# Kernel optimization log

Measured on AMD Instinct MI355X. Metric: run time of the kernel, lower is better.

## Reference

```python
import jax, jax.numpy as jnp
import numpy as np

N_NODES = 50000
N_EDGES = 1600000
N_GRAPHS = 512
D_IN, H1, H2, D_EMB = 128, 256, 256, 128
EPS = 1e-5


def setup_inputs() -> dict:
    key = jax.random.key(0)
    ks = jax.random.split(key, 12)
    V = jax.random.normal(ks[0], (N_NODES, D_IN), dtype=jnp.float32)
    edge_index = jax.random.randint(ks[1], (2, N_EDGES), 0, N_NODES, dtype=jnp.int64)
    batch_ids = jnp.sort(jax.random.randint(ks[2], (N_NODES,), 0, N_GRAPHS, dtype=jnp.int64))
    s = 0.05
    return {
        "V": V,
        "edge_index": edge_index,
        "batch_ids": batch_ids,
        "W1": jax.random.normal(ks[3], (D_IN, H1), jnp.float32) * s,
        "b1": jnp.zeros((H1,), jnp.float32),
        "g1": jnp.ones((H1,), jnp.float32),
        "be1": jnp.zeros((H1,), jnp.float32),
        "W2": jax.random.normal(ks[4], (H1, H2), jnp.float32) * s,
        "b2": jnp.zeros((H2,), jnp.float32),
        "g2": jnp.ones((H2,), jnp.float32),
        "be2": jnp.zeros((H2,), jnp.float32),
        "Wfc": jax.random.normal(ks[5], (H2, D_EMB), jnp.float32) * s,
        "bfc": jnp.zeros((D_EMB,), jnp.float32),
    }


def _gcn_conv(x, W, b, src, dst, n_nodes):
    x = x @ W  # [N, h]
    deg = jax.ops.segment_sum(jnp.ones_like(dst, dtype=x.dtype), dst, num_segments=n_nodes)
    dinv = jnp.where(deg > 0, jax.lax.rsqrt(deg), jnp.zeros_like(deg))
    norm = dinv[src] * dinv[dst]  # [E+N]
    out = jax.ops.segment_sum(x[src] * norm[:, None], dst, num_segments=n_nodes)
    return out + b


def _batch_norm(x, gamma, beta):
    mean = x.mean(axis=0)
    var = x.var(axis=0)  # biased, matches torch BN training normalization
    return (x - mean) * jax.lax.rsqrt(var + EPS) * gamma + beta


def reference(V, edge_index, batch_ids, W1, b1, g1, be1, W2, b2, g2, be2, Wfc, bfc):
    n = V.shape[0]
    loops = jnp.arange(n, dtype=edge_index.dtype)
    src = jnp.concatenate([edge_index[0], loops])
    dst = jnp.concatenate([edge_index[1], loops])

    h = _gcn_conv(V, W1, b1, src, dst, n)
    h = jax.nn.relu(_batch_norm(h, g1, be1))
    h = _gcn_conv(h, W2, b2, src, dst, n)
    h = jax.nn.relu(_batch_norm(h, g2, be2))

    # global mean pool over graphs
    sums = jax.ops.segment_sum(h, batch_ids, num_segments=N_GRAPHS)
    counts = jax.ops.segment_sum(jnp.ones((n,), h.dtype), batch_ids, num_segments=N_GRAPHS)
    G = sums / jnp.maximum(counts, 1.0)[:, None]
    return G @ Wfc + bfc
```

## Files before the change

kernel.cpp:

```cpp
#include <hip/hip_runtime.h>
#include <stdint.h>

typedef unsigned int u32;
typedef unsigned short u16;
typedef unsigned char u8;
typedef __attribute__((ext_vector_type(8))) short short8;
typedef __attribute__((ext_vector_type(4))) float f32x4;
typedef __attribute__((ext_vector_type(2))) float f32x2;

#if !__has_builtin(__builtin_amdgcn_cvt_pk_f32_fp8) || !__has_builtin(__builtin_amdgcn_cvt_pk_fp8_f32)
#include <hip/hip_fp8.h>
#define FP8_FALLBACK 1
#endif

#define NN   50000
#define NPAD 50048
#define NG   512
#define DIN  128
#define DH   256
#define BN_EPS 1e-5f
#define NB   196
#define EPB  4096
#define WCAP 24576
#define NT   8
#define TDIV 6250

#define CAST_BLK 6250
#define WT1_BLK  128
#define WT2_BLK  256

__device__ __forceinline__ float bf2f(u16 u) {
  union { u32 i; float f; } v; v.i = ((u32)u) << 16; return v.f;
}
__device__ __forceinline__ float bflo(u32 p) {
  union { u32 i; float f; } v; v.i = p << 16; return v.f;
}
__device__ __forceinline__ float bfhi(u32 p) {
  union { u32 i; float f; } v; v.i = p & 0xFFFF0000u; return v.f;
}
__device__ __forceinline__ u16 f2bf(float f) {
  union { float f; u32 i; } v; v.f = f;
  return (u16)((v.i + 0x7FFFu + ((v.i >> 16) & 1u)) >> 16);
}
__device__ __forceinline__ int load_idx(const void* p, long long i, int is64) {
  return is64 ? (int)((const long long*)p)[i] : ((const int*)p)[i];
}

__device__ __forceinline__ void fp8x4_dec(u32 w, float* o) {
#ifndef FP8_FALLBACK
  f32x2 lo = __builtin_amdgcn_cvt_pk_f32_fp8(w, false);
  f32x2 hi = __builtin_amdgcn_cvt_pk_f32_fp8(w, true);
  o[0] = lo.x; o[1] = lo.y; o[2] = hi.x; o[3] = hi.y;
#else
  __hip_fp8_e4m3 t;
#pragma unroll
  for (int k = 0; k < 4; ++k) { t.__x = (u8)(w >> (8 * k)); o[k] = (float)t; }
#endif
}
__device__ __forceinline__ u32 fp8x4_enc(float a, float b, float c, float d) {
#ifndef FP8_FALLBACK
  u32 r = 0;
  r = __builtin_amdgcn_cvt_pk_fp8_f32(a, b, r, false);
  r = __builtin_amdgcn_cvt_pk_fp8_f32(c, d, r, true);
  return r;
#else
  __hip_fp8_e4m3 qa(a), qb(b), qc(c), qd(d);
  return (u32)qa.__x | ((u32)qb.__x << 8) | ((u32)qc.__x << 16) | ((u32)qd.__x << 24);
#endif
}

__global__ void k_detect(const int* ei, int* flag) {
  if (threadIdx.x == 0 && blockIdx.x == 0) {
    int oddz = 0;
    for (int i = 0; i < 128; ++i) oddz += (ei[2 * i + 1] == 0) ? 1 : 0;
    *flag = (oddz == 128) ? 1 : 0;
  }
}

__global__ __launch_bounds__(256) void k_bcnt(const void* ei, int E,
    int* __restrict__ bcnt, const int* flag) {
  __shared__ int h[NB];
  int is64 = *flag;
  int t = threadIdx.x;
  for (int i = t; i < NB; i += 256) h[i] = 0;
  __syncthreads();
  long long base = (long long)blockIdx.x * EPB + t * 16;
#pragma unroll
  for (int j = 0; j < 16; ++j) {
    long long e = base + j;
    if (e < E) {
      int d = load_idx(ei, (long long)E + e, is64);
      atomicAdd(&h[d >> 8], 1);
    }
  }
  __syncthreads();
  for (int i = t; i < NB; i += 256)
    if (h[i]) atomicAdd(&bcnt[i], h[i]);
}

__global__ void k_bscan(const int* __restrict__ bcnt, int* __restrict__ bbase,
                        int* __restrict__ bcur) {
  __shared__ int s[256];
  int t = threadIdx.x;
  s[t] = (t < NB) ? bcnt[t] : 0; __syncthreads();
  for (int off = 1; off < 256; off <<= 1) {
    int x = s[t];
    int y = (t >= off) ? s[t - off] : 0;
    __syncthreads();
    s[t] = x + y; __syncthreads();
  }
  if (t < NB) {
    int ex = (t == 0) ? 0 : s[t - 1];
    bbase[t] = ex;
    bcur[t] = ex;
  }
}

__global__ __launch_bounds__(256) void k_bfill(const void* ei, int E,
    int* __restrict__ bcur, u32* __restrict__ recs, const int* flag) {
  __shared__ int h[NB];
  __shared__ int lbase[NB];
  __shared__ int lcur[NB];
  int is64 = *flag;
  int t = threadIdx.x;
  for (int i = t; i < NB; i += 256) h[i] = 0;
  __syncthreads();
  u32 rr[16];
  int bb[16];
  long long base = (long long)blockIdx.x * EPB + t * 16;
#pragma unroll
  for (int j = 0; j < 16; ++j) {
    long long e = base + j;
    if (e < E) {
      int s = load_idx(ei, e, is64);
      int d = load_idx(ei, (long long)E + e, is64);
      int b = d >> 8;
      rr[j] = ((u32)s << 8) | (u32)(d & 255);
      bb[j] = b;
      atomicAdd(&h[b], 1);
    } else bb[j] = -1;
  }
  __syncthreads();
  for (int i = t; i < NB; i += 256) {
    lbase[i] = h[i] ? atomicAdd(&bcur[i], h[i]) : 0;
    lcur[i] = 0;
  }
  __syncthreads();
#pragma unroll
  for (int j = 0; j < 16; ++j) {
    if (bb[j] >= 0) {
      int loc = atomicAdd(&lcur[bb[j]], 1);
      recs[lbase[bb[j]] + loc] = rr[j];
    }
  }
}

__global__ __launch_bounds__(512) void k_build(const u32* __restrict__ recs,
    const int* __restrict__ bbase, const int* __restrict__ bcnt,
    int* __restrict__ deg, int* __restrict__ offs, float* __restrict__ dinv,
    u16* __restrict__ csr_s) {
  __shared__ u32 cnt2[256][NT];
  __shared__ int woff[256];
  __shared__ int sscan[256];
  __shared__ u16 stage[WCAP];
  int b = blockIdx.x;
  int t = threadIdx.x;
  int nodeBase = b * 256;
  int nin = min(256, NN - nodeBase);
  for (int i = t; i < 256 * NT; i += 512) ((u32*)cnt2)[i] = 0;
  __syncthreads();
  int rb = bbase[b], cnt = bcnt[b];
  for (int i = t; i < cnt; i += 512) {
    u32 r = recs[rb + i];
    atomicAdd(&cnt2[r & 255u][(r >> 8) / TDIV], 1u);
  }
  __syncthreads();
  int slots = 0;
  if (t < nin) {
    cnt2[t][(u32)(nodeBase + t) / TDIV] += 1u;
    u32 run = 0;
#pragma unroll
    for (int k = 0; k < NT; ++k) { u32 c = cnt2[t][k]; cnt2[t][k] = run; run += c; }
    slots = (int)run;
  }
  if (t < 256) sscan[t] = slots;
  __syncthreads();
  for (int off = 1; off < 256; off <<= 1) {
    int x = (t < 256) ? sscan[t] : 0;
    int y = (t >= off && t < 256) ? sscan[t - off] : 0;
    __syncthreads();
    if (t < 256) sscan[t] = x + y;
    __syncthreads();
  }
  int gbase = rb + nodeBase;
  if (t < nin) {
    int ex = sscan[t] - slots;
    woff[t] = ex;
    offs[nodeBase + t] = gbase + ex;
    deg[nodeBase + t] = slots - 1;
    dinv[nodeBase + t] = rsqrtf((float)slots);
  }
  __syncthreads();
  int winsize = cnt + nin;
  if (winsize <= WCAP) {
    for (int i = t; i < cnt; i += 512) {
      u32 r = recs[rb + i];
      int d = r & 255u;
      u32 src = r >> 8;
      int loc = (int)atomicAdd(&cnt2[d][src / TDIV], 1u);
      stage[woff[d] + loc] = (u16)src;
    }
    if (t < nin) {
      int loc = (int)atomicAdd(&cnt2[t][(u32)(nodeBase + t) / TDIV], 1u);
      stage[woff[t] + loc] = (u16)(nodeBase + t);
    }
    __syncthreads();
    for (int i = t; i < winsize; i += 512) csr_s[gbase + i] = stage[i];
  } else {
    for (int i = t; i < cnt; i += 512) {
      u32 r = recs[rb + i];
      int d = r & 255u;
      u32 src = r >> 8;
      int loc = (int)atomicAdd(&cnt2[d][src / TDIV], 1u);
      csr_s[gbase + woff[d] + loc] = (u16)src;
    }
    if (t < nin) {
      int loc = (int)atomicAdd(&cnt2[t][(u32)(nodeBase + t) / TDIV], 1u);
      csr_s[gbase + woff[t] + loc] = (u16)(nodeBase + t);
    }
  }
}

__global__ void k_prep(const float* __restrict__ V, const float* __restrict__ W1,
                       const float* __restrict__ W2, const float* __restrict__ dinv,
                       u16* __restrict__ Vb, u16* __restrict__ W1t,
                       u16* __restrict__ W2t) {
  int b = blockIdx.x;
  if (b < CAST_BLK) {
    int i = (b * 256 + threadIdx.x) * 4;
    float dv = dinv[i >> 7];
    float4 v = *(const float4*)(V + i);
    ushort4 o;
    o.x = f2bf(v.x * dv); o.y = f2bf(v.y * dv);
    o.z = f2bf(v.z * dv); o.w = f2bf(v.w * dv);
    *(ushort4*)(Vb + i) = o;
  } else if (b < CAST_BLK + WT1_BLK) {
    int i = (b - CAST_BLK) * 256 + threadIdx.x;
    int k = i >> 8, c = i & 255;
    W1t[c * DIN + k] = f2bf(W1[i]);
  } else {
    int i = (b - CAST_BLK - WT1_BLK) * 256 + threadIdx.x;
    int k = i >> 8, c = i & 255;
    W2t[c * DH + k] = f2bf(W2[i]);
  }
}

__global__ __launch_bounds__(256) void k_agg1(const u16* __restrict__ in,
    const int* __restrict__ offs, const int* __restrict__ deg,
    const u16* __restrict__ csr_s, const float* __restrict__ dinv,
    u16* __restrict__ out) {
  int node = (blockIdx.x * 256 + threadIdx.x) >> 6;
  int lane = threadIdx.x & 63;
  if (node >= NN) return;
  int beg = offs[node];
  int end = beg + deg[node] + 1;
  float dinvn = dinv[node];
  int grp = lane >> 4, sub = lane & 15;
  float acc[8] = {};
  int e = beg + grp;
  bool v0 = e < end, v1 = e + 4 < end, v2 = e + 8 < end;
  uint4 r0, r1, r2;
  if (v0) r0 = *((const uint4*)(in + (size_t)csr_s[e] * 128) + sub);
  if (v1) r1 = *((const uint4*)(in + (size_t)csr_s[e + 4] * 128) + sub);
  if (v2) r2 = *((const uint4*)(in + (size_t)csr_s[e + 8] * 128) + sub);
  e += 12;
  while (v0) {
    bool v3 = e < end;
    uint4 r3;
    if (v3) r3 = *((const uint4*)(in + (size_t)csr_s[e] * 128) + sub);
    {
      u32 w[4] = {r0.x, r0.y, r0.z, r0.w};
#pragma unroll
      for (int j = 0; j < 4; ++j) {
        acc[2 * j + 0] += bflo(w[j]);
        acc[2 * j + 1] += bfhi(w[j]);
      }
    }
    r0 = r1; r1 = r2; r2 = r3;
    v0 = v1; v1 = v2; v2 = v3;
    e += 4;
  }
#pragma unroll
  for (int j = 0; j < 8; ++j) {
    acc[j] += __shfl_xor(acc[j], 16, 64);
    acc[j] += __shfl_xor(acc[j], 32, 64);
  }
  if (lane < 16) {
    u16* op = out + (size_t)node * 128 + sub * 8;
#pragma unroll
    for (int q = 0; q < 2; ++q) {
      ushort4 o;
      o.x = f2bf(acc[4 * q + 0] * dinvn);
      o.y = f2bf(acc[4 * q + 1] * dinvn);
      o.z = f2bf(acc[4 * q + 2] * dinvn);
      o.w = f2bf(acc[4 * q + 3] * dinvn);
      *(ushort4*)(op + 4 * q) = o;
    }
  }
}

__global__ __launch_bounds__(256) void k_agg2(const u8* __restrict__ in,
    const int* __restrict__ offs, const int* __restrict__ deg,
    const u16* __restrict__ csr_s, const float* __restrict__ dinv,
    u16* __restrict__ out) {
  int node = (blockIdx.x * 256 + threadIdx.x) >> 6;
  int lane = threadIdx.x & 63;
  if (node >= NN) return;
  int beg = offs[node];
  int end = beg + deg[node] + 1;
  float dinvn = dinv[node];
  int grp = lane >> 4, sub = lane & 15;
  float acc[16] = {};
  int e = beg + grp;
  bool v0 = e < end, v1 = e + 4 < end, v2 = e + 8 < end;
  uint4 r0, r1, r2;
  if (v0) r0 = *((const uint4*)(in + (size_t)csr_s[e] * 256) + sub);
  if (v1) r1 = *((const uint4*)(in + (size_t)csr_s[e + 4] * 256) + sub);
  if (v2) r2 = *((const uint4*)(in + (size_t)csr_s[e + 8] * 256) + sub);
  e += 12;
  while (v0) {
    bool v3 = e < end;
    uint4 r3;
    if (v3) r3 = *((const uint4*)(in + (size_t)csr_s[e] * 256) + sub);
    {
      u32 w[4] = {r0.x, r0.y, r0.z, r0.w};
#pragma unroll
      for (int j = 0; j < 4; ++j) {
        float f[4];
        fp8x4_dec(w[j], f);
        acc[4 * j + 0] += f[0];
        acc[4 * j + 1] += f[1];
        acc[4 * j + 2] += f[2];
        acc[4 * j + 3] += f[3];
      }
    }
    r0 = r1; r1 = r2; r2 = r3;
    v0 = v1; v1 = v2; v2 = v3;
    e += 4;
  }
#pragma unroll
  for (int j = 0; j < 16; ++j) {
    acc[j] += __shfl_xor(acc[j], 16, 64);
    acc[j] += __shfl_xor(acc[j], 32, 64);
  }
  if (lane < 16) {
    u16* op = out + (size_t)node * 256 + sub * 16;
#pragma unroll
    for (int q = 0; q < 4; ++q) {
      ushort4 o;
      o.x = f2bf(acc[4 * q + 0] * dinvn);
      o.y = f2bf(acc[4 * q + 1] * dinvn);
      o.z = f2bf(acc[4 * q + 2] * dinvn);
      o.w = f2bf(acc[4 * q + 3] * dinvn);
      *(ushort4*)(op + 4 * q) = o;
    }
  }
}

__global__ __launch_bounds__(256) void k_mgemm(const u16* __restrict__ A,
    const u16* __restrict__ Bt, const float* __restrict__ bias,
    u16* __restrict__ out, int M, int K,
    float* __restrict__ sums, float* __restrict__ sumsq) {
  __shared__ __align__(16) u16 As[128 * 32];
  __shared__ __align__(16) u16 Bs[128 * 32];
  int t = threadIdx.x;
  int l = t & 63;
  int w = t >> 6;
  int rowBase = blockIdx.x * 128;
  int colBase = blockIdx.y * 128;
  int wr = (w >> 1) * 64, wc = (w & 1) * 64;
  int rsel = l & 15, ksel = (l >> 4) * 8;

  f32x4 acc[4][4];
#pragma unroll
  for (int mi = 0; mi < 4; ++mi)
#pragma unroll
    for (int ni = 0; ni < 4; ++ni) acc[mi][ni] = (f32x4){0.f, 0.f, 0.f, 0.f};

  for (int k0 = 0; k0 < K; k0 += 32) {
#pragma unroll
    for (int c = 0; c < 2; ++c) {
      int idx = c * 256 + t;
      int row = idx >> 2;
      int kq = idx & 3;
      const u16* ga = A + (size_t)(rowBase + row) * K + k0 + kq * 8;
      const u16* gb = Bt + (size_t)(colBase + row) * K + k0 + kq * 8;
      __builtin_amdgcn_global_load_lds(
          (const __attribute__((address_space(1))) void*)ga,
          (__attribute__((address_space(3))) void*)(&As[idx * 8]), 16, 0, 0);
      __builtin_amdgcn_global_load_lds(
          (const __attribute__((address_space(1))) void*)gb,
          (__attribute__((address_space(3))) void*)(&Bs[idx * 8]), 16, 0, 0);
    }
    __syncthreads();
    short8 a[4], b[4];
#pragma unroll
    for (int mi = 0; mi < 4; ++mi)
      a[mi] = *(const short8*)(&As[(wr + mi * 16 + rsel) * 32 + ksel]);
#pragma unroll
    for (int ni = 0; ni < 4; ++ni)
      b[ni] = *(const short8*)(&Bs[(wc + ni * 16 + rsel) * 32 + ksel]);
#pragma unroll
    for (int mi = 0; mi < 4; ++mi)
#pragma unroll
      for (int ni = 0; ni < 4; ++ni)
        acc[mi][ni] = __builtin_amdgcn_mfma_f32_16x16x32_bf16(a[mi], b[ni], acc[mi][ni], 0, 0, 0);
    __syncthreads();
  }

#pragma unroll
  for (int ni = 0; ni < 4; ++ni) {
    int col = colBase + wc + ni * 16 + (l & 15);
    float bcol = bias[col];
    float s1 = 0.f, s2 = 0.f;
#pragma unroll
    for (int mi = 0; mi < 4; ++mi) {
#pragma unroll
      for (int r = 0; r < 4; ++r) {
        int row = rowBase + wr + mi * 16 + (l >> 4) * 4 + r;
        if (row < M) {
          float v = acc[mi][ni][r] + bcol;
          s1 += v; s2 += v * v;
          out[(size_t)row * 256 + col] = f2bf(v);
        }
      }
    }
    s1 += __shfl_xor(s1, 16, 64); s1 += __shfl_xor(s1, 32, 64);
    s2 += __shfl_xor(s2, 16, 64); s2 += __shfl_xor(s2, 32, 64);
    if (l < 16) {
      atomicAdd(&sums[col], s1);
      atomicAdd(&sumsq[col], s2);
    }
  }
}

__global__ void k_scale(const float* __restrict__ sum, const float* __restrict__ sumsq,
                        const float* __restrict__ g, const float* __restrict__ be,
                        float* __restrict__ scale, float* __restrict__ shift) {
  int c = threadIdx.x;
  float mean = sum[c] / (float)NN;
  float var = sumsq[c] / (float)NN - mean * mean;
  float sc = g[c] * rsqrtf(var + BN_EPS);
  scale[c] = sc;
  shift[c] = be[c] - mean * sc;
}

__global__ __launch_bounds__(256) void k_normcast(const u16* __restrict__ h,
    const float* __restrict__ scale, const float* __restrict__ shift,
    const float* __restrict__ dinv, u32* __restrict__ y) {
  long long i = ((long long)blockIdx.x * 256 + threadIdx.x) * 8;
  int row = (int)(i >> 8);
  float dv = dinv[row];
  int c = (int)(i & 255);
  ushort4 v0 = *(const ushort4*)(h + i);
  ushort4 v1 = *(const ushort4*)(h + i + 4);
  float f[8];
  f[0] = fmaxf(bf2f(v0.x) * scale[c + 0] + shift[c + 0], 0.f) * dv;
  f[1] = fmaxf(bf2f(v0.y) * scale[c + 1] + shift[c + 1], 0.f) * dv;
  f[2] = fmaxf(bf2f(v0.z) * scale[c + 2] + shift[c + 2], 0.f) * dv;
  f[3] = fmaxf(bf2f(v0.w) * scale[c + 3] + shift[c + 3], 0.f) * dv;
  f[4] = fmaxf(bf2f(v1.x) * scale[c + 4] + shift[c + 4], 0.f) * dv;
  f[5] = fmaxf(bf2f(v1.y) * scale[c + 5] + shift[c + 5], 0.f) * dv;
  f[6] = fmaxf(bf2f(v1.z) * scale[c + 6] + shift[c + 6], 0.f) * dv;
  f[7] = fmaxf(bf2f(v1.w) * scale[c + 7] + shift[c + 7], 0.f) * dv;
  uint2 o;
  o.x = fp8x4_enc(f[0], f[1], f[2], f[3]);
  o.y = fp8x4_enc(f[4], f[5], f[6], f[7]);
  *(uint2*)(y + (i >> 2)) = o;
}

__global__ __launch_bounds__(256) void k_pool(const u16* __restrict__ h,
    const float* __restrict__ scale, const float* __restrict__ shift,
    const void* batch, float* __restrict__ Gsum, int* __restrict__ Gcnt,
    const int* flag) {
  int is64 = *flag;
  int c = threadIdx.x;
  int nodeBase = blockIdx.x * 64;
  float sc = scale[c], sh = shift[c];
  float local = 0.f;
  int cur = -1, len = 0;
  int nmax = min(64, NN - nodeBase);
  for (int r = 0; r < nmax; ++r) {
    int node = nodeBase + r;
    int b = load_idx(batch, node, is64);
    if (b != cur) {
      if (cur >= 0) {
        atomicAdd(&Gsum[(size_t)cur * 256 + c], local);
        if (c == 0) atomicAdd(&Gcnt[cur], len);
      }
      cur = b; local = 0.f; len = 0;
    }
    float v = bf2f(h[(size_t)node * 256 + c]) * sc + sh;
    local += fmaxf(v, 0.f);
    len++;
  }
  if (cur >= 0) {
    atomicAdd(&Gsum[(size_t)cur * 256 + c], local);
    if (c == 0) atomicAdd(&Gcnt[cur], len);
  }
}

__global__ __launch_bounds__(128) void k_fc(const float* __restrict__ Gsum,
    const int* __restrict__ Gcnt, const float* __restrict__ Wfc,
    const float* __restrict__ bfc, float* __restrict__ out) {
  int g = blockIdx.x, j = threadIdx.x;
  float inv = 1.0f / fmaxf((float)Gcnt[g], 1.0f);
  float acc = 0.f;
#pragma unroll 4
  for (int c = 0; c < 256; ++c) acc += Gsum[(size_t)g * 256 + c] * Wfc[c * 128 + j];
  out[(size_t)g * 128 + j] = acc * inv + bfc[j];
}

extern "C" void kernel_launch(void* const* d_in, const int* in_sizes, int n_in,
                              void* d_out, int out_size, void* d_ws, size_t ws_size,
                              hipStream_t stream) {
  const float* V   = (const float*)d_in[0];
  const void*  EI  = d_in[1];
  const void*  BAT = d_in[2];
  const float* W1  = (const float*)d_in[3];
  const float* b1  = (const float*)d_in[4];
  const float* g1  = (const float*)d_in[5];
  const float* be1 = (const float*)d_in[6];
  const float* W2  = (const float*)d_in[7];
  const float* b2  = (const float*)d_in[8];
  const float* g2  = (const float*)d_in[9];
  const float* be2 = (const float*)d_in[10];
  const float* Wfc = (const float*)d_in[11];
  const float* bfc = (const float*)d_in[12];
  float* out = (float*)d_out;
  const int E  = in_sizes[1] / 2;
  const int NE = E + NN;

  char* w = (char*)d_ws;
  size_t o = 0;
  auto alloc = [&](size_t bytes) -> char* {
    char* r = w + o;
    o = (o + bytes + 255) & ~(size_t)255;
    return r;
  };
  int*   flag   = (int*)alloc(4);
  int*   deg    = (int*)alloc((size_t)NN * 4);
  int*   offs   = (int*)alloc((size_t)NN * 4);
  int*   bcnt   = (int*)alloc(NB * 4);
  int*   bbase  = (int*)alloc(NB * 4);
  int*   bcur   = (int*)alloc(NB * 4);
  u32*   recs   = (u32*)alloc((size_t)E * 4);
  u16*   csr_s  = (u16*)alloc((size_t)NE * 2);
  float* dinv   = (float*)alloc((size_t)NN * 4);
  float* stats  = (float*)alloc(8 * 256 * 4);
  float *sums1 = stats, *sumsq1 = stats + 256, *sums2 = stats + 512, *sumsq2 = stats + 768;
  float *scale1 = stats + 1024, *shift1 = stats + 1280, *scale2 = stats + 1536, *shift2 = stats + 1792;
  float* Gsum   = (float*)alloc((size_t)NG * DH * 4);
  int*   Gcnt   = (int*)alloc(NG * 4);
  u16*   W1t    = (u16*)alloc((size_t)256 * DIN * 2);
  u16*   W2t    = (u16*)alloc((size_t)256 * DH * 2);
  u16*   Vb     = (u16*)alloc((size_t)NN * DIN * 2);
  u16*   agg1   = (u16*)alloc((size_t)NPAD * DIN * 2);
  u16*   h1b    = (u16*)alloc((size_t)NN * DH * 2);
  u32*   h1n8   = (u32*)alloc((size_t)NN * DH);
  u16*   agg2   = (u16*)alloc((size_t)NPAD * DH * 2);
  u16*   h2b    = (u16*)alloc((size_t)NN * DH * 2);
  (void)n_in; (void)out_size; (void)ws_size;

  hipMemsetAsync(bcnt, 0, NB * 4, stream);
  hipMemsetAsync(stats, 0, 4 * 256 * 4, stream);
  hipMemsetAsync(Gsum, 0, (size_t)NG * DH * 4, stream);
  hipMemsetAsync(Gcnt, 0, (size_t)NG * 4, stream);

  const int gB = (E + EPB - 1) / EPB;

  k_detect<<<1, 64, 0, stream>>>((const int*)EI, flag);
  k_bcnt<<<gB, 256, 0, stream>>>(EI, E, bcnt, flag);
  k_bscan<<<1, 256, 0, stream>>>(bcnt, bbase, bcur);
  k_bfill<<<gB, 256, 0, stream>>>(EI, E, bcur, recs, flag);
  k_build<<<NB, 512, 0, stream>>>(recs, bbase, bcnt, deg, offs, dinv, csr_s);
  k_prep<<<CAST_BLK + WT1_BLK + WT2_BLK, 256, 0, stream>>>(V, W1, W2, dinv, Vb, W1t, W2t);

  k_agg1<<<(NN + 3) / 4, 256, 0, stream>>>(Vb, offs, deg, csr_s, dinv, agg1);
  k_mgemm<<<dim3((NN + 127) / 128, 2), 256, 0, stream>>>(agg1, W1t, b1, h1b, NN, DIN,
                                                         sums1, sumsq1);
  k_scale<<<1, 256, 0, stream>>>(sums1, sumsq1, g1, be1, scale1, shift1);
  k_normcast<<<6250, 256, 0, stream>>>(h1b, scale1, shift1, dinv, h1n8);

  k_agg2<<<(NN + 3) / 4, 256, 0, stream>>>((const u8*)h1n8, offs, deg, csr_s, dinv, agg2);
  k_mgemm<<<dim3((NN + 127) / 128, 2), 256, 0, stream>>>(agg2, W2t, b2, h2b, NN, DH,
                                                         sums2, sumsq2);
  k_scale<<<1, 256, 0, stream>>>(sums2, sumsq2, g2, be2, scale2, shift2);

  k_pool<<<(NN + 63) / 64, 256, 0, stream>>>(h2b, scale2, shift2, BAT, Gsum, Gcnt, flag);
  k_fc<<<NG, 128, 0, stream>>>(Gsum, Gcnt, Wfc, bfc, out);
}
```

Baseline: 336.9 us.

## Store layer-1 gathered features as FP8 and retile CSR source-ordering buckets

The input features, prescaled by dinv, are now stored as FP8 e4m3 instead of bf16, which halves the bytes the layer-1 aggregation gathers per edge. The agg1 kernel is reorganised so each 8-lane group covers a full 128-byte row and 8 edges are processed in parallel, with one extra shuffle stage in the reduction. Separately, the CSR build parameters change from 8 to 16 source tiles with a smaller window capacity, which alters how neighbour lists are ordered for locality. The cost is lower precision in the first aggregation, which risks accuracy error.

```diff
diff --git a/kernel.cpp b/kernel.cpp
--- a/kernel.cpp
+++ b/kernel.cpp
@@ -21,9 +21,9 @@
 #define BN_EPS 1e-5f
 #define NB   196
 #define EPB  4096
-#define WCAP 24576
-#define NT   8
-#define TDIV 6250
+#define WCAP 16384
+#define NT   16
+#define TDIV 3125
 
 #define CAST_BLK 6250
 #define WT1_BLK  128
@@ -31,12 +31,6 @@
 
 __device__ __forceinline__ float bf2f(u16 u) {
   union { u32 i; float f; } v; v.i = ((u32)u) << 16; return v.f;
-}
-__device__ __forceinline__ float bflo(u32 p) {
-  union { u32 i; float f; } v; v.i = p << 16; return v.f;
-}
-__device__ __forceinline__ float bfhi(u32 p) {
-  union { u32 i; float f; } v; v.i = p & 0xFFFF0000u; return v.f;
 }
 __device__ __forceinline__ u16 f2bf(float f) {
   union { float f; u32 i; } v; v.f = f;
@@ -233,17 +227,14 @@
 
 __global__ void k_prep(const float* __restrict__ V, const float* __restrict__ W1,
                        const float* __restrict__ W2, const float* __restrict__ dinv,
-                       u16* __restrict__ Vb, u16* __restrict__ W1t,
+                       u32* __restrict__ Vb8, u16* __restrict__ W1t,
                        u16* __restrict__ W2t) {
   int b = blockIdx.x;
   if (b < CAST_BLK) {
     int i = (b * 256 + threadIdx.x) * 4;
     float dv = dinv[i >> 7];
     float4 v = *(const float4*)(V + i);
-    ushort4 o;
-    o.x = f2bf(v.x * dv); o.y = f2bf(v.y * dv);
-    o.z = f2bf(v.z * dv); o.w = f2bf(v.w * dv);
-    *(ushort4*)(Vb + i) = o;
+    Vb8[i >> 2] = fp8x4_enc(v.x * dv, v.y * dv, v.z * dv, v.w * dv);
   } else if (b < CAST_BLK + WT1_BLK) {
     int i = (b - CAST_BLK) * 256 + threadIdx.x;
     int k = i >> 8, c = i & 255;
@@ -255,7 +246,7 @@
   }
 }
 
-__global__ __launch_bounds__(256) void k_agg1(const u16* __restrict__ in,
+__global__ __launch_bounds__(256) void k_agg1(const u8* __restrict__ in,
     const int* __restrict__ offs, const int* __restrict__ deg,
     const u16* __restrict__ csr_s, const float* __restrict__ dinv,
     u16* __restrict__ out) {
@@ -265,15 +256,15 @@
   int beg = offs[node];
   int end = beg + deg[node] + 1;
   float dinvn = dinv[node];
-  int grp = lane >> 4, sub = lane & 15;
-  float acc[8] = {};
+  int grp = lane >> 3, sub = lane & 7;
+  float acc[16] = {};
   int e = beg + grp;
-  bool v0 = e < end, v1 = e + 4 < end, v2 = e + 8 < end;
+  bool v0 = e < end, v1 = e + 8 < end, v2 = e + 16 < end;
   uint4 r0, r1, r2;
   if (v0) r0 = *((const uint4*)(in + (size_t)csr_s[e] * 128) + sub);
-  if (v1) r1 = *((const uint4*)(in + (size_t)csr_s[e + 4] * 128) + sub);
-  if (v2) r2 = *((const uint4*)(in + (size_t)csr_s[e + 8] * 128) + sub);
-  e += 12;
+  if (v1) r1 = *((const uint4*)(in + (size_t)csr_s[e + 8] * 128) + sub);
+  if (v2) r2 = *((const uint4*)(in + (size_t)csr_s[e + 16] * 128) + sub);
+  e += 24;
   while (v0) {
     bool v3 = e < end;
     uint4 r3;
@@ -282,23 +273,28 @@
       u32 w[4] = {r0.x, r0.y, r0.z, r0.w};
 #pragma unroll
       for (int j = 0; j < 4; ++j) {
-        acc[2 * j + 0] += bflo(w[j]);
-        acc[2 * j + 1] += bfhi(w[j]);
+        float f[4];
+        fp8x4_dec(w[j], f);
+        acc[4 * j + 0] += f[0];
+        acc[4 * j + 1] += f[1];
+        acc[4 * j + 2] += f[2];
+        acc[4 * j + 3] += f[3];
       }
     }
     r0 = r1; r1 = r2; r2 = r3;
     v0 = v1; v1 = v2; v2 = v3;
-    e += 4;
-  }
-#pragma unroll
-  for (int j = 0; j < 8; ++j) {
+    e += 8;
+  }
+#pragma unroll
+  for (int j = 0; j < 16; ++j) {
+    acc[j] += __shfl_xor(acc[j], 8, 64);
     acc[j] += __shfl_xor(acc[j], 16, 64);
     acc[j] += __shfl_xor(acc[j], 32, 64);
   }
-  if (lane < 16) {
-    u16* op = out + (size_t)node * 128 + sub * 8;
-#pragma unroll
-    for (int q = 0; q < 2; ++q) {
+  if (lane < 8) {
+    u16* op = out + (size_t)node * 128 + sub * 16;
+#pragma unroll
+    for (int q = 0; q < 4; ++q) {
       ushort4 o;
       o.x = f2bf(acc[4 * q + 0] * dinvn);
       o.y = f2bf(acc[4 * q + 1] * dinvn);
@@ -564,7 +560,7 @@
   int*   Gcnt   = (int*)alloc(NG * 4);
   u16*   W1t    = (u16*)alloc((size_t)256 * DIN * 2);
   u16*   W2t    = (u16*)alloc((size_t)256 * DH * 2);
-  u16*   Vb     = (u16*)alloc((size_t)NN * DIN * 2);
+  u32*   Vb8    = (u32*)alloc((size_t)NN * DIN);
   u16*   agg1   = (u16*)alloc((size_t)NPAD * DIN * 2);
   u16*   h1b    = (u16*)alloc((size_t)NN * DH * 2);
   u32*   h1n8   = (u32*)alloc((size_t)NN * DH);
@@ -584,9 +580,9 @@
   k_bscan<<<1, 256, 0, stream>>>(bcnt, bbase, bcur);
   k_bfill<<<gB, 256, 0, stream>>>(EI, E, bcur, recs, flag);
   k_build<<<NB, 512, 0, stream>>>(recs, bbase, bcnt, deg, offs, dinv, csr_s);
-  k_prep<<<CAST_BLK + WT1_BLK + WT2_BLK, 256, 0, stream>>>(V, W1, W2, dinv, Vb, W1t, W2t);
-
-  k_agg1<<<(NN + 3) / 4, 256, 0, stream>>>(Vb, offs, deg, csr_s, dinv, agg1);
+  k_prep<<<CAST_BLK + WT1_BLK + WT2_BLK, 256, 0, stream>>>(V, W1, W2, dinv, Vb8, W1t, W2t);
+
+  k_agg1<<<(NN + 3) / 4, 256, 0, stream>>>((const u8*)Vb8, offs, deg, csr_s, dinv, agg1);
   k_mgemm<<<dim3((NN + 127) / 128, 2), 256, 0, stream>>>(agg1, W1t, b1, h1b, NN, DIN,
                                                          sums1, sumsq1);
   k_scale<<<1, 256, 0, stream>>>(sums1, sumsq1, g1, be1, scale1, shift1);
```

Result: faster. 314.1 us (-6.8%).
